# Kernel tuning notes

Measured on AMD Instinct MI355X. Metric: run time of the kernel, lower is better.

The kernel has to match this reference:

```python
import jax, jax.numpy as jnp
import numpy as np

B, N, C, H = 4, 1024, 1024, 16
D = C // H                      # head_dim = 64
FFH = int(int(C * 4.0) * 2 / 3) # 2730
EPS = 1e-6


def rmsnorm(x, w):
    return w * (x * jax.lax.rsqrt(jnp.mean(x * x, axis=-1, keepdims=True) + EPS))


def setup_inputs() -> dict:
    key = jax.random.key(0)
    ks = jax.random.split(key, 12)
    s = 0.02
    return {
        "x": jax.random.normal(ks[0], (B, N, C), jnp.float32),
        "c": jax.random.normal(ks[1], (B, C), jnp.float32),
        "norm1_w": jnp.ones((C,), jnp.float32),
        "norm2_w": jnp.ones((C,), jnp.float32),
        "qkv_w": jax.random.normal(ks[2], (3 * C, C), jnp.float32) * s,
        "qkv_b": jnp.zeros((3 * C,), jnp.float32),
        "q_norm_w": jnp.ones((D,), jnp.float32),
        "k_norm_w": jnp.ones((D,), jnp.float32),
        "proj_w": jax.random.normal(ks[3], (C, C), jnp.float32) * s,
        "proj_b": jnp.zeros((C,), jnp.float32),
        "w12_w": jax.random.normal(ks[4], (2 * FFH, C), jnp.float32) * s,
        "w12_b": jnp.zeros((2 * FFH,), jnp.float32),
        "w3_w": jax.random.normal(ks[5], (C, FFH), jnp.float32) * s,
        "w3_b": jnp.zeros((C,), jnp.float32),
        "ada_w": jax.random.normal(ks[6], (6 * C, C), jnp.float32) * s,
        "ada_b": jnp.zeros((6 * C,), jnp.float32),
    }


def modulate(x, shift, scale):
    return x * (1.0 + scale[:, None, :]) + shift[:, None, :]


def attention(x, qkv_w, qkv_b, q_norm_w, k_norm_w, proj_w, proj_b):
    qkv = x @ qkv_w.T + qkv_b                       # (B,N,3C)
    qkv = qkv.reshape(B, N, 3, H, D)
    q, k, v = qkv[:, :, 0], qkv[:, :, 1], qkv[:, :, 2]   # (B,N,H,D)
    q = jnp.transpose(q, (0, 2, 1, 3))              # (B,H,N,D)
    k = jnp.transpose(k, (0, 2, 1, 3))
    v = jnp.transpose(v, (0, 2, 1, 3))
    q = rmsnorm(q, q_norm_w)
    k = rmsnorm(k, k_norm_w)
    attn = jnp.einsum("bhnd,bhmd->bhnm", q, k) / jnp.sqrt(jnp.float32(D))
    attn = jax.nn.softmax(attn, axis=-1)
    out = jnp.einsum("bhnm,bhmd->bhnd", attn, v)
    out = jnp.transpose(out, (0, 2, 1, 3)).reshape(B, N, C)
    return out @ proj_w.T + proj_b


def swiglu(x, w12_w, w12_b, w3_w, w3_b):
    x12 = x @ w12_w.T + w12_b                       # (B,N,2*FFH)
    x1, x2 = x12[..., :FFH], x12[..., FFH:]
    h = jax.nn.silu(x1) * x2
    return h @ w3_w.T + w3_b


def reference(x, c, norm1_w, norm2_w, qkv_w, qkv_b, q_norm_w, k_norm_w,
              proj_w, proj_b, w12_w, w12_b, w3_w, w3_b, ada_w, ada_b):
    ada = jax.nn.silu(c) @ ada_w.T + ada_b          # (B,6C)
    s1, g1, b1, s2, g2, b2 = jnp.split(ada, 6, axis=-1)
    a = attention(modulate(rmsnorm(x, norm1_w), s1, g1),
                  qkv_w, qkv_b, q_norm_w, k_norm_w, proj_w, proj_b)
    x = x + b1[:, None, :] * a
    m = swiglu(modulate(rmsnorm(x, norm2_w), s2, g2), w12_w, w12_b, w3_w, w3_b)
    x = x + b2[:, None, :] * m
    return x
```

## Files before the change

kernel.cpp:

```cpp
#include <hip/hip_runtime.h>

typedef short s16x8 __attribute__((ext_vector_type(8)));
typedef short s16x4 __attribute__((ext_vector_type(4)));
typedef float f32x4 __attribute__((ext_vector_type(4)));

#define B_   4
#define N_   1024
#define C_   1024
#define H_   16
#define D_   64
#define FFH_ 2730
#define FFP_ 2752
#define M_   4096

__device__ __forceinline__ short f2bf(float f) {
  unsigned u = __float_as_uint(f);
  u += 0x7fff + ((u >> 16) & 1);
  return (short)(unsigned short)(u >> 16);
}
__device__ __forceinline__ float silu(float x) { return x / (1.f + __expf(-x)); }

__global__ void cvt_bf(const float* __restrict__ s, short* __restrict__ d, const int n4) {
  for (int i = blockIdx.x * 256 + threadIdx.x; i < n4; i += gridDim.x * 256) {
    const float4 v = ((const float4*)s)[i];
    s16x4 o;
    o[0] = f2bf(v.x); o[1] = f2bf(v.y); o[2] = f2bf(v.z); o[3] = f2bf(v.w);
    *(s16x4*)(d + (size_t)i * 4) = o;
  }
}

__global__ void cvt_w3(const float* __restrict__ s, short* __restrict__ d) {
  const int col = blockIdx.x * 256 + threadIdx.x;
  const int row = blockIdx.y;
  if (col < FFP_)
    d[(size_t)row * FFP_ + col] = (col < FFH_) ? f2bf(s[(size_t)row * FFH_ + col]) : (short)0;
}

__global__ void ada_gemm(const float* __restrict__ c, const float* __restrict__ aw,
                         const float* __restrict__ ab, float* __restrict__ ada) {
  const int j = blockIdx.x;
  const int l = threadIdx.x;
  float acc[4] = {0.f, 0.f, 0.f, 0.f};
  const float4* wr = (const float4*)(aw + (size_t)j * 1024);
  #pragma unroll
  for (int p = 0; p < 4; ++p) {
    const float4 wv = wr[p * 64 + l];
    #pragma unroll
    for (int b = 0; b < 4; ++b) {
      const float4 cv = ((const float4*)(c + b * 1024))[p * 64 + l];
      acc[b] += silu(cv.x) * wv.x + silu(cv.y) * wv.y + silu(cv.z) * wv.z + silu(cv.w) * wv.w;
    }
  }
  #pragma unroll
  for (int b = 0; b < 4; ++b) {
    float a = acc[b];
    #pragma unroll
    for (int m = 1; m < 64; m <<= 1) a += __shfl_xor(a, m);
    if (l == 0) ada[b * 6144 + j] = a + ab[j];
  }
}

__global__ void rmsmod(const float* __restrict__ x, const float* __restrict__ wn,
                       const float* __restrict__ ada, const int sOff, const int gOff,
                       short* __restrict__ out) {
  const int row = blockIdx.x;
  const int b = row >> 10;
  const int t = threadIdx.x;
  const float4 v = ((const float4*)(x + (size_t)row * 1024))[t];
  float ss = v.x * v.x + v.y * v.y + v.z * v.z + v.w * v.w;
  #pragma unroll
  for (int m = 1; m < 64; m <<= 1) ss += __shfl_xor(ss, m);
  __shared__ float red[4];
  if ((t & 63) == 0) red[t >> 6] = ss;
  __syncthreads();
  const float rs = rsqrtf((red[0] + red[1] + red[2] + red[3]) * (1.f / 1024.f) + 1e-6f);
  const int j = t * 4;
  const float* sp = ada + b * 6144 + sOff + j;
  const float* gp = ada + b * 6144 + gOff + j;
  s16x4 o;
  o[0] = f2bf(v.x * rs * wn[j + 0] * (1.f + gp[0]) + sp[0]);
  o[1] = f2bf(v.y * rs * wn[j + 1] * (1.f + gp[1]) + sp[1]);
  o[2] = f2bf(v.z * rs * wn[j + 2] * (1.f + gp[2]) + sp[2]);
  o[3] = f2bf(v.w * rs * wn[j + 3] * (1.f + gp[3]) + sp[3]);
  *(s16x4*)(out + (size_t)row * 1024 + j) = o;
}

template <int EPI>
__launch_bounds__(256, 2)
__global__ void gemm_bt(const short* __restrict__ A, const short* __restrict__ Bt,
                        const int K, const int ldo,
                        const float* __restrict__ bias,
                        const float* __restrict__ adav,
                        const float* __restrict__ resid,
                        float* __restrict__ outF) {
  __shared__ short As[128 * 64];
  __shared__ short Bs[128 * 64];
  const int t = threadIdx.x;
  const int l = t & 63;
  const int w = t >> 6;
  const int wr = (w >> 1) * 64, wc = (w & 1) * 64;
  const int m0 = blockIdx.y * 128;
  const int n0 = blockIdx.x * 128;
  const int nT = K >> 6;
  const int sr = t >> 1;
  const int sc = (t & 1) * 4;

  f32x4 acc[4][4];
  const f32x4 z4 = {0.f, 0.f, 0.f, 0.f};
  #pragma unroll
  for (int i = 0; i < 4; ++i)
    #pragma unroll
    for (int j = 0; j < 4; ++j) acc[i][j] = z4;

  const short* gA = A + (size_t)(m0 + sr) * K + sc * 8;
  const short* gB = Bt + (size_t)(n0 + sr) * K + sc * 8;

  s16x8 ra[4], rb[4];
  #pragma unroll
  for (int p = 0; p < 4; ++p) {
    ra[p] = *(const s16x8*)(gA + p * 8);
    rb[p] = *(const s16x8*)(gB + p * 8);
  }

  for (int kt = 0; kt < nT; ++kt) {
    if (kt) __syncthreads();
    #pragma unroll
    for (int p = 0; p < 4; ++p) {
      const int cs = ((sc + p) ^ (sr & 7)) << 3;
      *(s16x8*)&As[sr * 64 + cs] = ra[p];
      *(s16x8*)&Bs[sr * 64 + cs] = rb[p];
    }
    __syncthreads();
    if (kt + 1 < nT) {
      const int ko = (kt + 1) * 64;
      #pragma unroll
      for (int p = 0; p < 4; ++p) {
        ra[p] = *(const s16x8*)(gA + ko + p * 8);
        rb[p] = *(const s16x8*)(gB + ko + p * 8);
      }
    }
    #pragma unroll
    for (int kk = 0; kk < 2; ++kk) {
      const int c16 = kk * 4 + (l >> 4);
      s16x8 af[4], bfr[4];
      #pragma unroll
      for (int mf = 0; mf < 4; ++mf) {
        const int r = wr + mf * 16 + (l & 15);
        af[mf] = *(const s16x8*)&As[r * 64 + ((c16 ^ (r & 7)) << 3)];
      }
      #pragma unroll
      for (int nf = 0; nf < 4; ++nf) {
        const int r = wc + nf * 16 + (l & 15);
        bfr[nf] = *(const s16x8*)&Bs[r * 64 + ((c16 ^ (r & 7)) << 3)];
      }
      #pragma unroll
      for (int mf = 0; mf < 4; ++mf)
        #pragma unroll
        for (int nf = 0; nf < 4; ++nf)
          acc[mf][nf] = __builtin_amdgcn_mfma_f32_16x16x32_bf16(af[mf], bfr[nf], acc[mf][nf], 0, 0, 0);
    }
  }

  const int bIdx = m0 >> 10;
  #pragma unroll
  for (int mf = 0; mf < 4; ++mf) {
    const int row = m0 + wr + mf * 16 + ((l >> 4) << 2);
    #pragma unroll
    for (int nf = 0; nf < 4; ++nf) {
      const int col = n0 + wc + nf * 16 + (l & 15);
      const float bsv = bias[col];
      #pragma unroll
      for (int i = 0; i < 4; ++i) {
        float v = acc[mf][nf][i] + bsv;
        if (EPI == 1)
          v = resid[(size_t)(row + i) * 1024 + col] + adav[bIdx * 6144 + col] * v;
        outF[(size_t)(row + i) * ldo + col] = v;
      }
    }
  }
}

__launch_bounds__(256, 2)
__global__ void gemm_w12(const short* __restrict__ A, const short* __restrict__ Bt,
                         const float* __restrict__ bias, short* __restrict__ outH) {
  __shared__ short As[128 * 64];
  __shared__ short B1s[64 * 64];
  __shared__ short B2s[64 * 64];
  const int t = threadIdx.x;
  const int l = t & 63;
  const int w = t >> 6;
  const int wr = (w >> 1) * 64, wc = (w & 1) * 32;
  const int m0 = blockIdx.y * 128;
  const int n0 = blockIdx.x * 64;
  const int sr = t >> 1, sc = (t & 1) * 4;
  const int sr2 = t >> 2, sc2 = (t & 3) * 2;
  const int jr = (n0 + sr2 < FFH_) ? (n0 + sr2) : (FFH_ - 1);

  f32x4 a1[4][2], a2[4][2];
  const f32x4 z4 = {0.f, 0.f, 0.f, 0.f};
  #pragma unroll
  for (int i = 0; i < 4; ++i)
    #pragma unroll
    for (int j = 0; j < 2; ++j) { a1[i][j] = z4; a2[i][j] = z4; }

  const short* gA = A + (size_t)(m0 + sr) * 1024 + sc * 8;
  const short* gB1 = Bt + (size_t)jr * 1024 + sc2 * 8;
  const short* gB2 = Bt + (size_t)(jr + FFH_) * 1024 + sc2 * 8;

  s16x8 ra[4], rb1[2], rb2[2];
  #pragma unroll
  for (int p = 0; p < 4; ++p) ra[p] = *(const s16x8*)(gA + p * 8);
  #pragma unroll
  for (int p = 0; p < 2; ++p) { rb1[p] = *(const s16x8*)(gB1 + p * 8); rb2[p] = *(const s16x8*)(gB2 + p * 8); }

  for (int kt = 0; kt < 16; ++kt) {
    if (kt) __syncthreads();
    #pragma unroll
    for (int p = 0; p < 4; ++p)
      *(s16x8*)&As[sr * 64 + (((sc + p) ^ (sr & 7)) << 3)] = ra[p];
    #pragma unroll
    for (int p = 0; p < 2; ++p) {
      const int cs = ((sc2 + p) ^ (sr2 & 7)) << 3;
      *(s16x8*)&B1s[sr2 * 64 + cs] = rb1[p];
      *(s16x8*)&B2s[sr2 * 64 + cs] = rb2[p];
    }
    __syncthreads();
    if (kt < 15) {
      const int ko = (kt + 1) * 64;
      #pragma unroll
      for (int p = 0; p < 4; ++p) ra[p] = *(const s16x8*)(gA + ko + p * 8);
      #pragma unroll
      for (int p = 0; p < 2; ++p) { rb1[p] = *(const s16x8*)(gB1 + ko + p * 8); rb2[p] = *(const s16x8*)(gB2 + ko + p * 8); }
    }
    #pragma unroll
    for (int kk = 0; kk < 2; ++kk) {
      const int c16 = kk * 4 + (l >> 4);
      s16x8 af[4], b1f[2], b2f[2];
      #pragma unroll
      for (int mf = 0; mf < 4; ++mf) {
        const int r = wr + mf * 16 + (l & 15);
        af[mf] = *(const s16x8*)&As[r * 64 + ((c16 ^ (r & 7)) << 3)];
      }
      #pragma unroll
      for (int nf = 0; nf < 2; ++nf) {
        const int r = wc + nf * 16 + (l & 15);
        const int idx = r * 64 + ((c16 ^ (r & 7)) << 3);
        b1f[nf] = *(const s16x8*)&B1s[idx];
        b2f[nf] = *(const s16x8*)&B2s[idx];
      }
      #pragma unroll
      for (int mf = 0; mf < 4; ++mf)
        #pragma unroll
        for (int nf = 0; nf < 2; ++nf) {
          a1[mf][nf] = __builtin_amdgcn_mfma_f32_16x16x32_bf16(af[mf], b1f[nf], a1[mf][nf], 0, 0, 0);
          a2[mf][nf] = __builtin_amdgcn_mfma_f32_16x16x32_bf16(af[mf], b2f[nf], a2[mf][nf], 0, 0, 0);
        }
    }
  }

  #pragma unroll
  for (int mf = 0; mf < 4; ++mf) {
    const int row = m0 + wr + mf * 16 + ((l >> 4) << 2);
    #pragma unroll
    for (int nf = 0; nf < 2; ++nf) {
      const int col = n0 + wc + nf * 16 + (l & 15);
      if (col < FFP_) {
        const bool real = col < FFH_;
        const float bb1 = real ? bias[col] : 0.f;
        const float bb2 = real ? bias[col + FFH_] : 0.f;
        #pragma unroll
        for (int i = 0; i < 4; ++i) {
          float o = 0.f;
          if (real) {
            const float v1 = a1[mf][nf][i] + bb1;
            const float v2 = a2[mf][nf][i] + bb2;
            o = silu(v1) * v2;
          }
          outH[(size_t)(row + i) * FFP_ + col] = f2bf(o);
        }
      }
    }
  }
}

__global__ void qk_post(const float* __restrict__ qkvf, const float* __restrict__ qnw,
                        const float* __restrict__ knw, short* __restrict__ qb,
                        short* __restrict__ kb) {
  const int gw = blockIdx.x * 4 + (threadIdx.x >> 6);
  const int l = threadIdx.x & 63;
  const int h = gw & 15, n = (gw >> 4) & 1023, b = gw >> 14;
  const size_t base = (size_t)(b * 1024 + n) * 3072 + h * 64 + l;
  const float qv = qkvf[base];
  const float kv = qkvf[base + 1024];
  float sq = qv * qv, sk = kv * kv;
  #pragma unroll
  for (int m = 1; m < 64; m <<= 1) { sq += __shfl_xor(sq, m); sk += __shfl_xor(sk, m); }
  const float rq = rsqrtf(sq * (1.f / 64.f) + 1e-6f);
  const float rk = rsqrtf(sk * (1.f / 64.f) + 1e-6f);
  const size_t o = ((size_t)(b * 16 + h) * 1024 + n) * 64 + l;
  qb[o] = f2bf(qv * rq * qnw[l] * 0.125f);
  kb[o] = f2bf(kv * rk * knw[l]);
}

__global__ void v_trans(const float* __restrict__ qkvf, short* __restrict__ vt) {
  __shared__ float ld[64][65];
  const int t = threadIdx.x;
  const int bh = blockIdx.y, b = bh >> 4, h = bh & 15;
  const int n0 = blockIdx.x * 64;
  const int nl = t >> 2, cb = (t & 3) * 16;
  const float* src = qkvf + (size_t)(b * 1024 + n0 + nl) * 3072 + 2048 + h * 64 + cb;
  #pragma unroll
  for (int p = 0; p < 16; ++p) ld[nl][cb + p] = src[p];
  __syncthreads();
  const int d = t >> 2, np = (t & 3) * 16;
  short* dst = vt + (size_t)(bh * 64 + d) * 1024 + n0 + np;
  #pragma unroll
  for (int p = 0; p < 16; ++p) dst[p] = f2bf(ld[np + p][d]);
}

__launch_bounds__(256, 2)
__global__ void attn(const short* __restrict__ qb, const short* __restrict__ kb,
                     const short* __restrict__ vt, short* __restrict__ ob) {
  __shared__ short Ks[64 * 64];
  __shared__ short Vs[64 * 64];
  __shared__ short Pl[4][32 * 64];
  const int t = threadIdx.x, l = t & 63, w = t >> 6;
  const int bh = blockIdx.y, b = bh >> 4, h = bh & 15;
  const int q0 = blockIdx.x * 128 + w * 32;
  const short* qp = qb + (size_t)bh * (N_ * D_);
  const short* kp = kb + (size_t)bh * (N_ * D_);
  const short* vp = vt + (size_t)bh * (D_ * N_);

  s16x8 qf[2][2];
  #pragma unroll
  for (int mf = 0; mf < 2; ++mf)
    #pragma unroll
    for (int kk = 0; kk < 2; ++kk)
      qf[mf][kk] = *(const s16x8*)&qp[(q0 + mf * 16 + (l & 15)) * 64 + kk * 32 + ((l >> 4) * 8)];

  f32x4 aco[2][4];
  float rm[2][4], rl[2][4];
  const f32x4 z4 = {0.f, 0.f, 0.f, 0.f};
  #pragma unroll
  for (int mf = 0; mf < 2; ++mf) {
    #pragma unroll
    for (int nd = 0; nd < 4; ++nd) aco[mf][nd] = z4;
    #pragma unroll
    for (int i = 0; i < 4; ++i) { rm[mf][i] = -1e30f; rl[mf][i] = 0.f; }
  }

  const int sr = t >> 2, sc = (t & 3) * 2;
  s16x8 rk[2], rv[2];
  #pragma unroll
  for (int p = 0; p < 2; ++p) {
    rk[p] = *(const s16x8*)&kp[sr * 64 + (sc + p) * 8];
    rv[p] = *(const s16x8*)&vp[sr * 1024 + (sc + p) * 8];
  }

  for (int kt = 0; kt < 16; ++kt) {
    if (kt) __syncthreads();
    #pragma unroll
    for (int p = 0; p < 2; ++p) {
      const int cs = ((sc + p) ^ (sr & 7)) << 3;
      *(s16x8*)&Ks[sr * 64 + cs] = rk[p];
      *(s16x8*)&Vs[sr * 64 + cs] = rv[p];
    }
    __syncthreads();
    if (kt < 15) {
      const int kv0 = (kt + 1) * 64;
      #pragma unroll
      for (int p = 0; p < 2; ++p) {
        rk[p] = *(const s16x8*)&kp[(kv0 + sr) * 64 + (sc + p) * 8];
        rv[p] = *(const s16x8*)&vp[sr * 1024 + kv0 + (sc + p) * 8];
      }
    }

    f32x4 s[2][4];
    #pragma unroll
    for (int mf = 0; mf < 2; ++mf)
      #pragma unroll
      for (int nf = 0; nf < 4; ++nf) s[mf][nf] = z4;

    #pragma unroll
    for (int kk = 0; kk < 2; ++kk) {
      const int c16 = kk * 4 + (l >> 4);
      s16x8 kf[4];
      #pragma unroll
      for (int nf = 0; nf < 4; ++nf) {
        const int r = nf * 16 + (l & 15);
        kf[nf] = *(const s16x8*)&Ks[r * 64 + ((c16 ^ (r & 7)) << 3)];
      }
      #pragma unroll
      for (int mf = 0; mf < 2; ++mf)
        #pragma unroll
        for (int nf = 0; nf < 4; ++nf)
          s[mf][nf] = __builtin_amdgcn_mfma_f32_16x16x32_bf16(qf[mf][kk], kf[nf], s[mf][nf], 0, 0, 0);
    }

    #pragma unroll
    for (int mf = 0; mf < 2; ++mf) {
      #pragma unroll
      for (int i = 0; i < 4; ++i) {
        float pm = fmaxf(fmaxf(s[mf][0][i], s[mf][1][i]), fmaxf(s[mf][2][i], s[mf][3][i]));
        pm = fmaxf(pm, __shfl_xor(pm, 1));
        pm = fmaxf(pm, __shfl_xor(pm, 2));
        pm = fmaxf(pm, __shfl_xor(pm, 4));
        pm = fmaxf(pm, __shfl_xor(pm, 8));
        const float nm = fmaxf(rm[mf][i], pm);
        const float corr = __expf(rm[mf][i] - nm);
        rm[mf][i] = nm;
        float rs = 0.f;
        #pragma unroll
        for (int nf = 0; nf < 4; ++nf) {
          const float p = __expf(s[mf][nf][i] - nm);
          s[mf][nf][i] = p;
          rs += p;
        }
        rs += __shfl_xor(rs, 1);
        rs += __shfl_xor(rs, 2);
        rs += __shfl_xor(rs, 4);
        rs += __shfl_xor(rs, 8);
        rl[mf][i] = rl[mf][i] * corr + rs;
        #pragma unroll
        for (int nd = 0; nd < 4; ++nd) aco[mf][nd][i] *= corr;
      }
    }

    short* pw = &Pl[w][0];
    #pragma unroll
    for (int mf = 0; mf < 2; ++mf)
      #pragma unroll
      for (int nf = 0; nf < 4; ++nf)
        #pragma unroll
        for (int i = 0; i < 4; ++i) {
          const int row = mf * 16 + ((l >> 4) << 2) + i;
          const int col = nf * 16 + (l & 15);
          pw[row * 64 + (((col >> 3) ^ (row & 7)) << 3) + (col & 7)] = f2bf(s[mf][nf][i]);
        }

    #pragma unroll
    for (int kk = 0; kk < 2; ++kk) {
      const int c16 = kk * 4 + (l >> 4);
      s16x8 vf[4];
      #pragma unroll
      for (int nd = 0; nd < 4; ++nd) {
        const int r = nd * 16 + (l & 15);
        vf[nd] = *(const s16x8*)&Vs[r * 64 + ((c16 ^ (r & 7)) << 3)];
      }
      #pragma unroll
      for (int mf = 0; mf < 2; ++mf) {
        const int pr = mf * 16 + (l & 15);
        const s16x8 pf = *(const s16x8*)&pw[pr * 64 + ((c16 ^ (pr & 7)) << 3)];
        #pragma unroll
        for (int nd = 0; nd < 4; ++nd)
          aco[mf][nd] = __builtin_amdgcn_mfma_f32_16x16x32_bf16(pf, vf[nd], aco[mf][nd], 0, 0, 0);
      }
    }
  }

  #pragma unroll
  for (int mf = 0; mf < 2; ++mf)
    #pragma unroll
    for (int i = 0; i < 4; ++i) {
      const float inv = 1.f / rl[mf][i];
      const int row = q0 + mf * 16 + ((l >> 4) << 2) + i;
      #pragma unroll
      for (int nd = 0; nd < 4; ++nd) {
        const int col = h * 64 + nd * 16 + (l & 15);
        ob[(size_t)(b * 1024 + row) * 1024 + col] = f2bf(aco[mf][nd][i] * inv);
      }
    }
}

extern "C" void kernel_launch(void* const* d_in, const int* in_sizes, int n_in,
                              void* d_out, int out_size, void* d_ws, size_t ws_size,
                              hipStream_t stream) {
  const float* x     = (const float*)d_in[0];
  const float* c     = (const float*)d_in[1];
  const float* n1w   = (const float*)d_in[2];
  const float* n2w   = (const float*)d_in[3];
  const float* qkvw  = (const float*)d_in[4];
  const float* qkvb  = (const float*)d_in[5];
  const float* qnw   = (const float*)d_in[6];
  const float* knw   = (const float*)d_in[7];
  const float* projw = (const float*)d_in[8];
  const float* projb = (const float*)d_in[9];
  const float* w12w  = (const float*)d_in[10];
  const float* w12b  = (const float*)d_in[11];
  const float* w3w   = (const float*)d_in[12];
  const float* w3b   = (const float*)d_in[13];
  const float* adaw  = (const float*)d_in[14];
  const float* adab  = (const float*)d_in[15];
  float* outp = (float*)d_out;

  char* ws = (char*)d_ws;
  size_t off = 0;
  auto alloc = [&](size_t bytes) { void* p = ws + off; off += (bytes + 255) & ~(size_t)255; return p; };
  short* WQKV = (short*)alloc(3072ull * 1024 * 2);
  short* WPROJ = (short*)alloc(1024ull * 1024 * 2);
  short* W12B = (short*)alloc(5460ull * 1024 * 2);
  short* W3B = (short*)alloc(1024ull * 2752 * 2);
  float* ADA = (float*)alloc(4ull * 6144 * 4);
  short* H1 = (short*)alloc(4096ull * 1024 * 2);
  float* QKVF = (float*)alloc(4096ull * 3072 * 4);
  short* QBF = (short*)alloc(64ull * 1024 * 64 * 2);
  short* KBF = (short*)alloc(64ull * 1024 * 64 * 2);
  short* VTB = (short*)alloc(64ull * 64 * 1024 * 2);
  short* OBF = (short*)alloc(4096ull * 1024 * 2);
  float* X1 = (float*)alloc(4096ull * 1024 * 4);
  short* H2 = (short*)alloc(4096ull * 1024 * 2);
  short* HB = (short*)alloc(4096ull * 2752 * 2);

  cvt_bf<<<2048, 256, 0, stream>>>(qkvw, WQKV, 3072 * 1024 / 4);
  cvt_bf<<<1024, 256, 0, stream>>>(projw, WPROJ, 1024 * 1024 / 4);
  cvt_bf<<<2048, 256, 0, stream>>>(w12w, W12B, 5460 * 1024 / 4);
  cvt_w3<<<dim3(11, 1024), 256, 0, stream>>>(w3w, W3B);
  ada_gemm<<<6144, 64, 0, stream>>>(c, adaw, adab, ADA);
  rmsmod<<<4096, 256, 0, stream>>>(x, n1w, ADA, 0, 1024, H1);
  gemm_bt<0><<<dim3(24, 32), 256, 0, stream>>>(H1, WQKV, 1024, 3072, qkvb, nullptr, nullptr, QKVF);
  qk_post<<<16384, 256, 0, stream>>>(QKVF, qnw, knw, QBF, KBF);
  v_trans<<<dim3(16, 64), 256, 0, stream>>>(QKVF, VTB);
  attn<<<dim3(8, 64), 256, 0, stream>>>(QBF, KBF, VTB, OBF);
  gemm_bt<1><<<dim3(8, 32), 256, 0, stream>>>(OBF, WPROJ, 1024, 1024, projb, ADA + 2048, x, X1);
  rmsmod<<<4096, 256, 0, stream>>>(X1, n2w, ADA, 3072, 4096, H2);
  gemm_w12<<<dim3(43, 32), 256, 0, stream>>>(H2, W12B, w12b, HB);
  gemm_bt<1><<<dim3(8, 32), 256, 0, stream>>>(HB, W3B, 2752, 1024, w3b, ADA + 5120, X1, outp);
}
```

Measured before the change: 293.1 us.

## Use direct global-to-LDS loads, XCD-aware tile remap, wider w12 tiles, MFMA priority

GEMM kernels now stage A/B tiles with global_load_lds (direct to shared memory, pre-swizzled addresses) instead of register prefetch plus LDS stores, which drops the register-level double buffering. Block indices are remapped so neighbouring tiles land on the same XCD for L2 reuse. The w12 GEMM tile widens from 64 to 128 columns with 32 accumulators per wave, halving the grid. s_setprio is raised around MFMA blocks in the GEMMs and attention. Losing the overlap between loading the next tile and computing the current one may expose memory latency, and the larger w12 tile raises register and LDS pressure.

```diff
diff --git a/kernel.cpp b/kernel.cpp
--- a/kernel.cpp
+++ b/kernel.cpp
@@ -19,6 +19,12 @@
   return (short)(unsigned short)(u >> 16);
 }
 __device__ __forceinline__ float silu(float x) { return x / (1.f + __expf(-x)); }
+
+__device__ __forceinline__ void gload16(const void* g, void* l) {
+  __builtin_amdgcn_global_load_lds(
+      (const __attribute__((address_space(1))) unsigned*)g,
+      (__attribute__((address_space(3))) unsigned*)l, 16, 0, 0);
+}
 
 __global__ void cvt_bf(const float* __restrict__ s, short* __restrict__ d, const int n4) {
   for (int i = blockIdx.x * 256 + threadIdx.x; i < n4; i += gridDim.x * 256) {
@@ -99,11 +105,13 @@
   const int l = t & 63;
   const int w = t >> 6;
   const int wr = (w >> 1) * 64, wc = (w & 1) * 64;
-  const int m0 = blockIdx.y * 128;
-  const int n0 = blockIdx.x * 128;
+
+  const int nwg = gridDim.x * gridDim.y;
+  int lin = blockIdx.y * gridDim.x + blockIdx.x;
+  lin = (lin & 7) * (nwg >> 3) + (lin >> 3);
+  const int m0 = (lin / gridDim.x) * 128;
+  const int n0 = (lin % gridDim.x) * 128;
   const int nT = K >> 6;
-  const int sr = t >> 1;
-  const int sc = (t & 1) * 4;
 
   f32x4 acc[4][4];
   const f32x4 z4 = {0.f, 0.f, 0.f, 0.f};
@@ -112,33 +120,22 @@
     #pragma unroll
     for (int j = 0; j < 4; ++j) acc[i][j] = z4;
 
-  const short* gA = A + (size_t)(m0 + sr) * K + sc * 8;
-  const short* gB = Bt + (size_t)(n0 + sr) * K + sc * 8;
-
-  s16x8 ra[4], rb[4];
-  #pragma unroll
-  for (int p = 0; p < 4; ++p) {
-    ra[p] = *(const s16x8*)(gA + p * 8);
-    rb[p] = *(const s16x8*)(gB + p * 8);
-  }
+  const int lr = l >> 3;
+  const int lc = (l & 7) ^ lr;
+  const short* gAs = A + (size_t)(m0 + w * 32 + lr) * K + lc * 8;
+  const short* gBs = Bt + (size_t)(n0 + w * 32 + lr) * K + lc * 8;
+  short* lA = As + (w * 32) * 64;
+  short* lB = Bs + (w * 32) * 64;
 
   for (int kt = 0; kt < nT; ++kt) {
     if (kt) __syncthreads();
+    const int ko = kt * 64;
     #pragma unroll
     for (int p = 0; p < 4; ++p) {
-      const int cs = ((sc + p) ^ (sr & 7)) << 3;
-      *(s16x8*)&As[sr * 64 + cs] = ra[p];
-      *(s16x8*)&Bs[sr * 64 + cs] = rb[p];
+      gload16(gAs + (size_t)p * 8 * K + ko, lA + p * 8 * 64);
+      gload16(gBs + (size_t)p * 8 * K + ko, lB + p * 8 * 64);
     }
     __syncthreads();
-    if (kt + 1 < nT) {
-      const int ko = (kt + 1) * 64;
-      #pragma unroll
-      for (int p = 0; p < 4; ++p) {
-        ra[p] = *(const s16x8*)(gA + ko + p * 8);
-        rb[p] = *(const s16x8*)(gB + ko + p * 8);
-      }
-    }
     #pragma unroll
     for (int kk = 0; kk < 2; ++kk) {
       const int c16 = kk * 4 + (l >> 4);
@@ -153,11 +150,13 @@
         const int r = wc + nf * 16 + (l & 15);
         bfr[nf] = *(const s16x8*)&Bs[r * 64 + ((c16 ^ (r & 7)) << 3)];
       }
+      __builtin_amdgcn_s_setprio(1);
       #pragma unroll
       for (int mf = 0; mf < 4; ++mf)
         #pragma unroll
         for (int nf = 0; nf < 4; ++nf)
           acc[mf][nf] = __builtin_amdgcn_mfma_f32_16x16x32_bf16(af[mf], bfr[nf], acc[mf][nf], 0, 0, 0);
+      __builtin_amdgcn_s_setprio(0);
     }
   }
 
@@ -184,77 +183,71 @@
 __global__ void gemm_w12(const short* __restrict__ A, const short* __restrict__ Bt,
                          const float* __restrict__ bias, short* __restrict__ outH) {
   __shared__ short As[128 * 64];
-  __shared__ short B1s[64 * 64];
-  __shared__ short B2s[64 * 64];
+  __shared__ short B1s[128 * 64];
+  __shared__ short B2s[128 * 64];
   const int t = threadIdx.x;
   const int l = t & 63;
   const int w = t >> 6;
-  const int wr = (w >> 1) * 64, wc = (w & 1) * 32;
-  const int m0 = blockIdx.y * 128;
-  const int n0 = blockIdx.x * 64;
-  const int sr = t >> 1, sc = (t & 1) * 4;
-  const int sr2 = t >> 2, sc2 = (t & 3) * 2;
-  const int jr = (n0 + sr2 < FFH_) ? (n0 + sr2) : (FFH_ - 1);
-
-  f32x4 a1[4][2], a2[4][2];
+  const int wr = (w >> 1) * 64, wc = (w & 1) * 64;
+
+  const int nwg = gridDim.x * gridDim.y;
+  int lin = blockIdx.y * gridDim.x + blockIdx.x;
+  lin = (lin & 7) * (nwg >> 3) + (lin >> 3);
+  const int m0 = (lin / gridDim.x) * 128;
+  const int n0 = (lin % gridDim.x) * 128;
+
+  f32x4 a1[4][4], a2[4][4];
   const f32x4 z4 = {0.f, 0.f, 0.f, 0.f};
   #pragma unroll
   for (int i = 0; i < 4; ++i)
     #pragma unroll
-    for (int j = 0; j < 2; ++j) { a1[i][j] = z4; a2[i][j] = z4; }
-
-  const short* gA = A + (size_t)(m0 + sr) * 1024 + sc * 8;
-  const short* gB1 = Bt + (size_t)jr * 1024 + sc2 * 8;
-  const short* gB2 = Bt + (size_t)(jr + FFH_) * 1024 + sc2 * 8;
-
-  s16x8 ra[4], rb1[2], rb2[2];
-  #pragma unroll
-  for (int p = 0; p < 4; ++p) ra[p] = *(const s16x8*)(gA + p * 8);
-  #pragma unroll
-  for (int p = 0; p < 2; ++p) { rb1[p] = *(const s16x8*)(gB1 + p * 8); rb2[p] = *(const s16x8*)(gB2 + p * 8); }
+    for (int j = 0; j < 4; ++j) { a1[i][j] = z4; a2[i][j] = z4; }
+
+  const int lr = l >> 3;
+  const int lc = (l & 7) ^ lr;
+  const short* gAs = A + (size_t)(m0 + w * 32 + lr) * 1024 + lc * 8;
+  const int rbase = n0 + w * 32 + lr;
+  short* lA = As + (w * 32) * 64;
+  short* lB1 = B1s + (w * 32) * 64;
+  short* lB2 = B2s + (w * 32) * 64;
 
   for (int kt = 0; kt < 16; ++kt) {
     if (kt) __syncthreads();
-    #pragma unroll
-    for (int p = 0; p < 4; ++p)
-      *(s16x8*)&As[sr * 64 + (((sc + p) ^ (sr & 7)) << 3)] = ra[p];
-    #pragma unroll
-    for (int p = 0; p < 2; ++p) {
-      const int cs = ((sc2 + p) ^ (sr2 & 7)) << 3;
-      *(s16x8*)&B1s[sr2 * 64 + cs] = rb1[p];
-      *(s16x8*)&B2s[sr2 * 64 + cs] = rb2[p];
+    const int ko = kt * 64;
+    #pragma unroll
+    for (int p = 0; p < 4; ++p) {
+      int j = rbase + p * 8;
+      if (j >= FFH_) j = FFH_ - 1;
+      gload16(gAs + (size_t)p * 8 * 1024 + ko, lA + p * 8 * 64);
+      gload16(Bt + (size_t)j * 1024 + ko + lc * 8, lB1 + p * 8 * 64);
+      gload16(Bt + (size_t)(j + FFH_) * 1024 + ko + lc * 8, lB2 + p * 8 * 64);
     }
     __syncthreads();
-    if (kt < 15) {
-      const int ko = (kt + 1) * 64;
-      #pragma unroll
-      for (int p = 0; p < 4; ++p) ra[p] = *(const s16x8*)(gA + ko + p * 8);
-      #pragma unroll
-      for (int p = 0; p < 2; ++p) { rb1[p] = *(const s16x8*)(gB1 + ko + p * 8); rb2[p] = *(const s16x8*)(gB2 + ko + p * 8); }
-    }
     #pragma unroll
     for (int kk = 0; kk < 2; ++kk) {
       const int c16 = kk * 4 + (l >> 4);
-      s16x8 af[4], b1f[2], b2f[2];
+      s16x8 af[4], b1f[4], b2f[4];
       #pragma unroll
       for (int mf = 0; mf < 4; ++mf) {
         const int r = wr + mf * 16 + (l & 15);
         af[mf] = *(const s16x8*)&As[r * 64 + ((c16 ^ (r & 7)) << 3)];
       }
       #pragma unroll
-      for (int nf = 0; nf < 2; ++nf) {
+      for (int nf = 0; nf < 4; ++nf) {
         const int r = wc + nf * 16 + (l & 15);
         const int idx = r * 64 + ((c16 ^ (r & 7)) << 3);
         b1f[nf] = *(const s16x8*)&B1s[idx];
         b2f[nf] = *(const s16x8*)&B2s[idx];
       }
+      __builtin_amdgcn_s_setprio(1);
       #pragma unroll
       for (int mf = 0; mf < 4; ++mf)
         #pragma unroll
-        for (int nf = 0; nf < 2; ++nf) {
+        for (int nf = 0; nf < 4; ++nf) {
           a1[mf][nf] = __builtin_amdgcn_mfma_f32_16x16x32_bf16(af[mf], b1f[nf], a1[mf][nf], 0, 0, 0);
           a2[mf][nf] = __builtin_amdgcn_mfma_f32_16x16x32_bf16(af[mf], b2f[nf], a2[mf][nf], 0, 0, 0);
         }
+      __builtin_amdgcn_s_setprio(0);
     }
   }
 
@@ -262,7 +255,7 @@
   for (int mf = 0; mf < 4; ++mf) {
     const int row = m0 + wr + mf * 16 + ((l >> 4) << 2);
     #pragma unroll
-    for (int nf = 0; nf < 2; ++nf) {
+    for (int nf = 0; nf < 4; ++nf) {
       const int col = n0 + wc + nf * 16 + (l & 15);
       if (col < FFP_) {
         const bool real = col < FFH_;
@@ -390,11 +383,13 @@
         const int r = nf * 16 + (l & 15);
         kf[nf] = *(const s16x8*)&Ks[r * 64 + ((c16 ^ (r & 7)) << 3)];
       }
+      __builtin_amdgcn_s_setprio(1);
       #pragma unroll
       for (int mf = 0; mf < 2; ++mf)
         #pragma unroll
         for (int nf = 0; nf < 4; ++nf)
           s[mf][nf] = __builtin_amdgcn_mfma_f32_16x16x32_bf16(qf[mf][kk], kf[nf], s[mf][nf], 0, 0, 0);
+      __builtin_amdgcn_s_setprio(0);
     }
 
     #pragma unroll
@@ -447,6 +442,7 @@
         const int r = nd * 16 + (l & 15);
         vf[nd] = *(const s16x8*)&Vs[r * 64 + ((c16 ^ (r & 7)) << 3)];
       }
+      __builtin_amdgcn_s_setprio(1);
       #pragma unroll
       for (int mf = 0; mf < 2; ++mf) {
         const int pr = mf * 16 + (l & 15);
@@ -455,6 +451,7 @@
         for (int nd = 0; nd < 4; ++nd)
           aco[mf][nd] = __builtin_amdgcn_mfma_f32_16x16x32_bf16(pf, vf[nd], aco[mf][nd], 0, 0, 0);
       }
+      __builtin_amdgcn_s_setprio(0);
     }
   }
 
@@ -523,6 +520,6 @@
   attn<<<dim3(8, 64), 256, 0, stream>>>(QBF, KBF, VTB, OBF);
   gemm_bt<1><<<dim3(8, 32), 256, 0, stream>>>(OBF, WPROJ, 1024, 1024, projb, ADA + 2048, x, X1);
   rmsmod<<<4096, 256, 0, stream>>>(X1, n2w, ADA, 3072, 4096, H2);
-  gemm_w12<<<dim3(43, 32), 256, 0, stream>>>(H2, W12B, w12b, HB);
+  gemm_w12<<<dim3(22, 32), 256, 0, stream>>>(H2, W12B, w12b, HB);
   gemm_bt<1><<<dim3(8, 32), 256, 0, stream>>>(HB, W3B, 2752, 1024, w3b, ADA + 5120, X1, outp);
 }
```

Result: no change. 295.4 us (+0.8%).
